# Kernel optimization log

Measured on AMD Instinct MI355X. Metric: run time of the kernel, lower is better.

The kernel has to match this reference:

```python
import jax, jax.numpy as jnp
import numpy as np

TEMPERATURE = 8.0  # sqrt(d_k=64)

def setup_inputs() -> dict:
    key = jax.random.key(0)
    kq, kk, kv, km1, km2 = jax.random.split(key, 5)
    B, Lq, Lk, D = 128, 512, 512, 64
    q = jax.random.normal(kq, (B, Lq, D), dtype=jnp.float32)
    k = jax.random.normal(kk, (B, Lk, D), dtype=jnp.float32)
    v = jax.random.normal(kv, (B, Lk, D), dtype=jnp.float32)
    key_mask = jax.random.bernoulli(km1, 0.5, (B, Lq, Lk))
    query_mask = jax.random.bernoulli(km2, 0.5, (B, Lq, Lk))
    return {"q": q, "k": k, "v": v, "key_mask": key_mask, "query_mask": query_mask}

def reference(q, k, v, key_mask, query_mask):
    # attn = (q @ k^T) / temperature, pre-softmax key masking with -inf
    scores = jnp.einsum('bqd,bkd->bqk', q, k) / TEMPERATURE
    scores = jnp.where(key_mask, -jnp.inf, scores)
    attn = jax.nn.softmax(scores, axis=-1)
    # post-softmax query-row zeroing
    attn = jnp.where(query_mask, 0.0, attn)
    # dropout omitted (eval mode / deterministic reference)
    output = jnp.einsum('bqk,bkd->bqd', attn, v)
    return (output, attn)
```

## Files before the change

kernel.cpp:

```cpp
#include <hip/hip_runtime.h>
#include <hip/hip_bf16.h>

#define BATCH 128
#define LQ    512
#define LK    512
#define DH    64
#define TQ    16
#define KC    128

#define KSTR  72
#define VSTR  136
#define SSTR  516
#define ASTR  520

typedef float  float4v __attribute__((ext_vector_type(4)));
typedef short  short8v __attribute__((ext_vector_type(8)));
typedef short  short4v __attribute__((ext_vector_type(4)));
typedef int    int4v   __attribute__((ext_vector_type(4)));

__device__ __forceinline__ short bf16r(float f) {
  union { float f; unsigned u; } x; x.f = f;
  unsigned r = x.u + 0x7FFFu + ((x.u >> 16) & 1u);
  return (short)(r >> 16);
}

__global__ __launch_bounds__(256)
void sdpa_kernel(const float* __restrict__ Q, const float* __restrict__ K,
                 const float* __restrict__ V, const int* __restrict__ KM,
                 const int* __restrict__ QM, float* __restrict__ OUT,
                 float* __restrict__ ATT)
{
  __shared__ short kvs[KC * KSTR];
  __shared__ float sc[TQ * SSTR];
  __shared__ short at[TQ * ASTR];

  const int b    = blockIdx.x >> 5;
  const int q0   = (blockIdx.x & 31) * TQ;
  const int tid  = threadIdx.x;
  const int lane = tid & 63;
  const int wave = tid >> 6;
  const int lm   = lane & 15;
  const int quad = lane >> 4;

  const float* qrow = Q + ((size_t)(b * LQ + q0 + lm)) * DH + quad * 8;
  short8v aq0, aq1;
  {
    float4v f0 = *(const float4v*)(qrow + 0);
    float4v f1 = *(const float4v*)(qrow + 4);
    float4v f2 = *(const float4v*)(qrow + 32);
    float4v f3 = *(const float4v*)(qrow + 36);
#pragma unroll
    for (int e = 0; e < 4; ++e) {
      aq0[e]     = bf16r(f0[e]);
      aq0[e + 4] = bf16r(f1[e]);
      aq1[e]     = bf16r(f2[e]);
      aq1[e + 4] = bf16r(f3[e]);
    }
  }

  for (int kt = 0; kt < LK / KC; ++kt) {
    const float* ksrc = K + ((size_t)(b * LK + kt * KC)) * DH;
#pragma unroll
    for (int i = 0; i < 8; ++i) {
      int fl = (tid + i * 256) << 2;
      int r  = fl >> 6, c = fl & 63;
      float4v d4 = *(const float4v*)(ksrc + fl);
      short4v s4;
      s4[0] = bf16r(d4[0]); s4[1] = bf16r(d4[1]);
      s4[2] = bf16r(d4[2]); s4[3] = bf16r(d4[3]);
      *(short4v*)&kvs[r * KSTR + c] = s4;
    }
    __syncthreads();
#pragma unroll
    for (int t = 0; t < 2; ++t) {
      int ntl = (wave * 2 + t) * 16;
      const short* bp = &kvs[(ntl + lm) * KSTR + quad * 8];
      short8v b0 = *(const short8v*)(bp);
      short8v b1 = *(const short8v*)(bp + 32);
      float4v acc = {0.f, 0.f, 0.f, 0.f};
      acc = __builtin_amdgcn_mfma_f32_16x16x32_bf16(aq0, b0, acc, 0, 0, 0);
      acc = __builtin_amdgcn_mfma_f32_16x16x32_bf16(aq1, b1, acc, 0, 0, 0);
      int n  = kt * KC + ntl + lm;
      int m0 = quad * 4;
      sc[(m0 + 0) * SSTR + n] = acc[0];
      sc[(m0 + 1) * SSTR + n] = acc[1];
      sc[(m0 + 2) * SSTR + n] = acc[2];
      sc[(m0 + 3) * SSTR + n] = acc[3];
    }
    __syncthreads();
  }

  const int row = tid >> 4;
  const int col = tid & 15;
  const size_t gro = (size_t)(b * LQ + q0 + row) * LK;
  const int* kmr = KM + gro;
  const int* qmr = QM + gro;
  float s[32];
  float mx = -INFINITY;
#pragma unroll
  for (int j = 0; j < 8; ++j) {
    int kk = col * 4 + j * 64;
    int4v  msk = *(const int4v*)(kmr + kk);
    float4v s4 = *(const float4v*)&sc[row * SSTR + kk];
#pragma unroll
    for (int e = 0; e < 4; ++e) {
      float val = msk[e] ? -INFINITY : s4[e];
      s[j * 4 + e] = val;
      mx = fmaxf(mx, val);
    }
  }
#pragma unroll
  for (int off = 8; off; off >>= 1) mx = fmaxf(mx, __shfl_xor(mx, off, 64));
  float sum = 0.f;
#pragma unroll
  for (int j = 0; j < 32; ++j) {
    float p = __expf((s[j] - mx) * 0.125f);
    s[j] = p;
    sum += p;
  }
#pragma unroll
  for (int off = 8; off; off >>= 1) sum += __shfl_xor(sum, off, 64);
  const float inv = 1.f / sum;
  float* arow = ATT + gro;
#pragma unroll
  for (int j = 0; j < 8; ++j) {
    int kk = col * 4 + j * 64;
    int4v qmk = *(const int4v*)(qmr + kk);
    float4v a4;
#pragma unroll
    for (int e = 0; e < 4; ++e)
      a4[e] = qmk[e] ? 0.f : s[j * 4 + e] * inv;
    *(float4v*)(arow + kk) = a4;
    short4v ab;
    ab[0] = bf16r(a4[0]); ab[1] = bf16r(a4[1]);
    ab[2] = bf16r(a4[2]); ab[3] = bf16r(a4[3]);
    *(short4v*)&at[row * ASTR + kk] = ab;
  }

  float4v oacc = {0.f, 0.f, 0.f, 0.f};
  for (int kt = 0; kt < LK / KC; ++kt) {
    const float* vsrc = V + ((size_t)(b * LK + kt * KC)) * DH;
#pragma unroll
    for (int i = 0; i < 8; ++i) {
      int fl = (tid + i * 256) << 2;
      int r = fl >> 6, c = fl & 63;
      float4v d4 = *(const float4v*)(vsrc + fl);
      kvs[(c + 0) * VSTR + r] = bf16r(d4[0]);
      kvs[(c + 1) * VSTR + r] = bf16r(d4[1]);
      kvs[(c + 2) * VSTR + r] = bf16r(d4[2]);
      kvs[(c + 3) * VSTR + r] = bf16r(d4[3]);
    }
    __syncthreads();
#pragma unroll
    for (int ks = 0; ks < 4; ++ks) {
      const short* ap = &at[lm * ASTR + kt * KC + ks * 32 + quad * 8];
      short8v a8 = *(const short8v*)ap;
      const short* bp = &kvs[(wave * 16 + lm) * VSTR + ks * 32 + quad * 8];
      short8v b8 = *(const short8v*)bp;
      oacc = __builtin_amdgcn_mfma_f32_16x16x32_bf16(a8, b8, oacc, 0, 0, 0);
    }
    __syncthreads();
  }
  {
    int m0 = quad * 4;
    float* obase = OUT + ((size_t)(b * LQ + q0 + m0)) * DH + wave * 16 + lm;
    obase[0 * DH] = oacc[0];
    obase[1 * DH] = oacc[1];
    obase[2 * DH] = oacc[2];
    obase[3 * DH] = oacc[3];
  }
}

extern "C" void kernel_launch(void* const* d_in, const int* in_sizes, int n_in,
                              void* d_out, int out_size, void* d_ws, size_t ws_size,
                              hipStream_t stream) {
  const float* q  = (const float*)d_in[0];
  const float* k  = (const float*)d_in[1];
  const float* v  = (const float*)d_in[2];
  const int*   km = (const int*)d_in[3];
  const int*   qm = (const int*)d_in[4];
  float* out  = (float*)d_out;
  float* attn = out + (size_t)BATCH * LQ * DH;
  dim3 grid(BATCH * (LQ / TQ));
  dim3 block(256);
  hipLaunchKernelGGL(sdpa_kernel, grid, block, 0, stream,
                     q, k, v, km, qm, out, attn);
}
```

Before: 422.9 us.

## Store scores as fp16 in shared memory, prefetch masks, swizzle V transpose

Scores are now kept in fp16 inside one shared buffer that is later reused for the bf16 attention tile. This roughly halves LDS use, and launch bounds now request 4 blocks per CU for higher occupancy. Key and query masks are loaded into registers early to hide global latency. The V transpose into LDS now writes 4-element packed chunks through an XOR swizzle instead of scalar strided stores, to cut bank conflicts. Rounding scores to fp16 before softmax loses precision and could exceed tolerance, and the extra registers for the masks may limit occupancy.

Result: faster. 378.5 us (-10.5%).

```diff
diff --git a/kernel.cpp b/kernel.cpp
--- a/kernel.cpp
+++ b/kernel.cpp
@@ -9,14 +9,14 @@
 #define KC    128
 
 #define KSTR  72
-#define VSTR  136
-#define SSTR  516
-#define ASTR  520
-
-typedef float  float4v __attribute__((ext_vector_type(4)));
-typedef short  short8v __attribute__((ext_vector_type(8)));
-typedef short  short4v __attribute__((ext_vector_type(4)));
-typedef int    int4v   __attribute__((ext_vector_type(4)));
+#define VROW  136
+#define SSTR  520
+
+typedef float    float4v __attribute__((ext_vector_type(4)));
+typedef short    short8v __attribute__((ext_vector_type(8)));
+typedef short    short4v __attribute__((ext_vector_type(4)));
+typedef int      int4v   __attribute__((ext_vector_type(4)));
+typedef _Float16 half4v  __attribute__((ext_vector_type(4)));
 
 __device__ __forceinline__ short bf16r(float f) {
   union { float f; unsigned u; } x; x.f = f;
@@ -24,15 +24,14 @@
   return (short)(r >> 16);
 }
 
-__global__ __launch_bounds__(256)
+__global__ __launch_bounds__(256, 4)
 void sdpa_kernel(const float* __restrict__ Q, const float* __restrict__ K,
                  const float* __restrict__ V, const int* __restrict__ KM,
                  const int* __restrict__ QM, float* __restrict__ OUT,
                  float* __restrict__ ATT)
 {
   __shared__ short kvs[KC * KSTR];
-  __shared__ float sc[TQ * SSTR];
-  __shared__ short at[TQ * ASTR];
+  __shared__ short scs[TQ * SSTR];
 
   const int b    = blockIdx.x >> 5;
   const int q0   = (blockIdx.x & 31) * TQ;
@@ -41,6 +40,15 @@
   const int wave = tid >> 6;
   const int lm   = lane & 15;
   const int quad = lane >> 4;
+
+  const int row = tid >> 4;
+  const int col = tid & 15;
+  const size_t gro = (size_t)(b * LQ + q0 + row) * LK;
+
+  int4v kmv[8];
+#pragma unroll
+  for (int j = 0; j < 8; ++j)
+    kmv[j] = *(const int4v*)(KM + gro + col * 4 + j * 64);
 
   const float* qrow = Q + ((size_t)(b * LQ + q0 + lm)) * DH + quad * 8;
   short8v aq0, aq1;
@@ -82,33 +90,29 @@
       acc = __builtin_amdgcn_mfma_f32_16x16x32_bf16(aq1, b1, acc, 0, 0, 0);
       int n  = kt * KC + ntl + lm;
       int m0 = quad * 4;
-      sc[(m0 + 0) * SSTR + n] = acc[0];
-      sc[(m0 + 1) * SSTR + n] = acc[1];
-      sc[(m0 + 2) * SSTR + n] = acc[2];
-      sc[(m0 + 3) * SSTR + n] = acc[3];
-    }
-    __syncthreads();
-  }
-
-  const int row = tid >> 4;
-  const int col = tid & 15;
-  const size_t gro = (size_t)(b * LQ + q0 + row) * LK;
-  const int* kmr = KM + gro;
-  const int* qmr = QM + gro;
+#pragma unroll
+      for (int j = 0; j < 4; ++j)
+        *(_Float16*)&scs[(m0 + j) * SSTR + n] = (_Float16)acc[j];
+    }
+    __syncthreads();
+  }
+
   float s[32];
   float mx = -INFINITY;
 #pragma unroll
   for (int j = 0; j < 8; ++j) {
-    int kk = col * 4 + j * 64;
-    int4v  msk = *(const int4v*)(kmr + kk);
-    float4v s4 = *(const float4v*)&sc[row * SSTR + kk];
+    half4v h4 = *(const half4v*)&scs[row * SSTR + col * 4 + j * 64];
 #pragma unroll
     for (int e = 0; e < 4; ++e) {
-      float val = msk[e] ? -INFINITY : s4[e];
+      float val = kmv[j][e] ? -INFINITY : (float)h4[e];
       s[j * 4 + e] = val;
       mx = fmaxf(mx, val);
     }
   }
+  int4v qmv[8];
+#pragma unroll
+  for (int j = 0; j < 8; ++j)
+    qmv[j] = *(const int4v*)(QM + gro + col * 4 + j * 64);
 #pragma unroll
   for (int off = 8; off; off >>= 1) mx = fmaxf(mx, __shfl_xor(mx, off, 64));
   float sum = 0.f;
@@ -125,38 +129,52 @@
 #pragma unroll
   for (int j = 0; j < 8; ++j) {
     int kk = col * 4 + j * 64;
-    int4v qmk = *(const int4v*)(qmr + kk);
     float4v a4;
 #pragma unroll
     for (int e = 0; e < 4; ++e)
-      a4[e] = qmk[e] ? 0.f : s[j * 4 + e] * inv;
+      a4[e] = qmv[j][e] ? 0.f : s[j * 4 + e] * inv;
     *(float4v*)(arow + kk) = a4;
     short4v ab;
     ab[0] = bf16r(a4[0]); ab[1] = bf16r(a4[1]);
     ab[2] = bf16r(a4[2]); ab[3] = bf16r(a4[3]);
-    *(short4v*)&at[row * ASTR + kk] = ab;
+    *(short4v*)&scs[row * SSTR + kk] = ab;
   }
 
   float4v oacc = {0.f, 0.f, 0.f, 0.f};
   for (int kt = 0; kt < LK / KC; ++kt) {
     const float* vsrc = V + ((size_t)(b * LK + kt * KC)) * DH;
 #pragma unroll
-    for (int i = 0; i < 8; ++i) {
-      int fl = (tid + i * 256) << 2;
-      int r = fl >> 6, c = fl & 63;
-      float4v d4 = *(const float4v*)(vsrc + fl);
-      kvs[(c + 0) * VSTR + r] = bf16r(d4[0]);
-      kvs[(c + 1) * VSTR + r] = bf16r(d4[1]);
-      kvs[(c + 2) * VSTR + r] = bf16r(d4[2]);
-      kvs[(c + 3) * VSTR + r] = bf16r(d4[3]);
+    for (int it = 0; it < 2; ++it) {
+      int Bx = tid + 256 * it;
+      int bR = Bx >> 4;
+      int bC = Bx & 15;
+      const float* vp = vsrc + bR * 4 * DH + bC * 4;
+      float4v r0 = *(const float4v*)(vp);
+      float4v r1 = *(const float4v*)(vp + DH);
+      float4v r2 = *(const float4v*)(vp + 2 * DH);
+      float4v r3 = *(const float4v*)(vp + 3 * DH);
+#pragma unroll
+      for (int e = 0; e < 4; ++e) {
+        int d  = bC * 4 + e;
+        int gp = bR ^ (d & 31);
+        short4v s4;
+        s4[0] = bf16r(r0[e]); s4[1] = bf16r(r1[e]);
+        s4[2] = bf16r(r2[e]); s4[3] = bf16r(r3[e]);
+        *(short4v*)&kvs[d * VROW + gp * 4] = s4;
+      }
     }
     __syncthreads();
 #pragma unroll
     for (int ks = 0; ks < 4; ++ks) {
-      const short* ap = &at[lm * ASTR + kt * KC + ks * 32 + quad * 8];
+      const short* ap = &scs[lm * SSTR + kt * KC + ks * 32 + quad * 8];
       short8v a8 = *(const short8v*)ap;
-      const short* bp = &kvs[(wave * 16 + lm) * VSTR + ks * 32 + quad * 8];
-      short8v b8 = *(const short8v*)bp;
+      int n  = wave * 16 + lm;
+      int g0 = ks * 8 + quad * 2;
+      short4v lo = *(const short4v*)&kvs[n * VROW + ((g0    ) ^ (n & 31)) * 4];
+      short4v hi = *(const short4v*)&kvs[n * VROW + ((g0 + 1) ^ (n & 31)) * 4];
+      short8v b8;
+      b8[0] = lo[0]; b8[1] = lo[1]; b8[2] = lo[2]; b8[3] = lo[3];
+      b8[4] = hi[0]; b8[5] = hi[1]; b8[6] = hi[2]; b8[7] = hi[3];
       oacc = __builtin_amdgcn_mfma_f32_16x16x32_bf16(a8, b8, oacc, 0, 0, 0);
     }
     __syncthreads();
```
